# Optimization experiments

Hardware: AMD Instinct MI355X
Metric: run time of the kernel (lower is better)

Reference implementation:

```python
import math
import jax, jax.numpy as jnp
import numpy as np

# ---------- static Cl(3,0,0) algebra tables ----------
_BLADES = [(), (1,), (2,), (3,), (1, 2), (1, 3), (2, 3), (1, 2, 3)]
N_BLADES = 8
SUBSPACES = np.array([1, 3, 3, 1])
GRADE = np.array([len(b) for b in _BLADES])  # blade index -> grade

def _blade_mul(a, b):
    idx = list(a) + list(b)
    sign = 1
    changed = True
    while changed:
        changed = False
        for t in range(len(idx) - 1):
            if idx[t] > idx[t + 1]:
                idx[t], idx[t + 1] = idx[t + 1], idx[t]
                sign = -sign
                changed = True
    out = []
    t = 0
    while t < len(idx):
        if t + 1 < len(idx) and idx[t] == idx[t + 1]:
            t += 2  # e_i e_i = +1 (Euclidean metric)
        else:
            out.append(idx[t]); t += 1
    return sign, tuple(out)

# cayley[i, j, k]: e_i * e_k contributes sign to blade j (matches einsum 'bni,nijk,bnk->bnj')
CAYLEY = np.zeros((N_BLADES, N_BLADES, N_BLADES), dtype=np.float32)
for i, ba in enumerate(_BLADES):
    for k, bb in enumerate(_BLADES):
        s, res = _blade_mul(ba, bb)
        CAYLEY[i, _BLADES.index(res), k] = s

_starts = np.concatenate([[0], np.cumsum(SUBSPACES)[:-1]])
_paths = np.zeros((4, 4, 4), dtype=bool)
for gi in range(4):
    for gj in range(4):
        for gk in range(4):
            si, sj, sk = _starts[gi], _starts[gj], _starts[gk]
            blk = CAYLEY[si:si + SUBSPACES[gi], sj:sj + SUBSPACES[gj], sk:sk + SUBSPACES[gk]]
            _paths[gi, gj, gk] = np.any(blk != 0)
_grade_idx = np.argwhere(_paths)  # row-major order, matches torch.nonzero
N_PATHS = len(_grade_idx)  # 20 for Cl(3,0)

_bi, _bj, _bk, _pidx, _cv = [], [], [], [], []
for p, (gi, gj, gk) in enumerate(_grade_idx):
    for bi in range(_starts[gi], _starts[gi] + SUBSPACES[gi]):
        for bj in range(_starts[gj], _starts[gj] + SUBSPACES[gj]):
            for bk in range(_starts[gk], _starts[gk] + SUBSPACES[gk]):
                c = CAYLEY[bi, bj, bk]
                if c != 0:
                    _bi.append(bi); _bj.append(bj); _bk.append(bk)
                    _pidx.append(p); _cv.append(c)
BI = np.array(_bi); BJ = np.array(_bj); BK = np.array(_bk)
PIDX = np.array(_pidx); CV = np.array(_cv, dtype=np.float32)  # E = 64 nonzero entries

G_ONEHOT = (GRADE[:, None] == np.arange(4)[None, :]).astype(np.float32)  # (8, 4)

B, N_IN, N_OUT = 2048, 512, 512
EPS = 1e-6

def setup_inputs() -> dict:
    key = jax.random.key(0)
    k = jax.random.split(key, 6)
    x = jax.random.normal(k[0], (B, N_IN, N_BLADES), jnp.float32)
    weight = jax.random.normal(k[1], (N_OUT, N_IN, N_PATHS), jnp.float32) / math.sqrt(N_IN * 4)
    w_right = jax.random.normal(k[2], (N_IN, N_IN, 4), jnp.float32) / math.sqrt(N_IN)
    w_left = jax.random.normal(k[3], (N_OUT, N_IN, 4), jnp.float32) / math.sqrt(N_IN)
    b_left = jax.random.normal(k[4], (N_OUT,), jnp.float32) * 0.01
    norm_a = jnp.zeros((1, N_IN, 4), jnp.float32)  # normalization_init = 0
    return dict(x=x, weight=weight, w_right=w_right, w_left=w_left, b_left=b_left, norm_a=norm_a)

def _mvlinear(x, w):
    # w: (out, in, n_grades) -> per-blade weight via grade lookup (repeat_interleave)
    return jnp.einsum('bni,mni->bmi', x, w[:, :, GRADE])

def reference(x, weight, w_right, w_left, b_left, norm_a):
    # linear_right (no bias)
    xr = _mvlinear(x, w_right)
    # NormalizationLayer: per-grade norm, sigmoid-gated rescale toward 1
    norms = jnp.sqrt(jnp.einsum('bni,ig->bng', xr * xr, G_ONEHOT))  # (B, n, 4)
    factor = jax.nn.sigmoid(norm_a) * (norms - 1.0) + 1.0
    xr = xr / (factor[:, :, GRADE] + EPS)
    # sparse bilinear geometric product: only the 64 nonzero cayley entries
    pair = x[:, :, BI] * xr[:, :, BK]            # (B, n, E)
    wsel = weight[:, :, PIDX] * CV               # (m, n, E)
    tmp = jnp.einsum('bne,mne->bme', pair, wsel)  # (B, m, E)
    bilinear = jnp.zeros((x.shape[0], weight.shape[0], N_BLADES), x.dtype).at[:, :, BJ].add(tmp)
    # linear_left with bias embedded on the scalar blade (index 0)
    left = _mvlinear(x, w_left).at[:, :, 0].add(b_left)
    return (left + bilinear) / math.sqrt(2.0)
```

## Files before the change

kernel.cpp:

```cpp
#include <hip/hip_runtime.h>
#include <stdint.h>


#define B_DIM 2048
#define N_DIM 512
#define PLANE (B_DIM * N_DIM)
#define WPLANE (N_DIM * N_DIM)
#define KTOT (9 * N_DIM)
#define LDSP 40

using frag8 = __attribute__((ext_vector_type(8))) short;
using f32x4 = __attribute__((ext_vector_type(4))) float;

__device__ __forceinline__ float bf2f(unsigned short u) {
  union { unsigned int i; float f; } v;
  v.i = ((unsigned int)u) << 16;
  return v.f;
}
__device__ __forceinline__ unsigned short f2bf(float f) {
  unsigned int u = __float_as_uint(f);
  return (unsigned short)((u + 0x7FFFu + ((u >> 16) & 1u)) >> 16);
}
__device__ __forceinline__ unsigned int pairpack(unsigned int a, unsigned int r) {
  const float pe = __uint_as_float(a << 16) * __uint_as_float(r << 16);
  const float po = __uint_as_float(a & 0xFFFF0000u) * __uint_as_float(r & 0xFFFF0000u);
  return __builtin_amdgcn_perm(__float_as_uint(po) + 0x8000u,
                               __float_as_uint(pe) + 0x8000u, 0x07060302u);
}

#define SGN_INIT {                                                     \
  {0,0,0,0,0x8000,0x8000,0x8000,0x8000},                               \
  {0,0,0,0,0x8000,0x8000,0x8000,0x8000},                               \
  {0,0x8000,0,0,0,0,0x8000,0},                                         \
  {0,0x8000,0x8000,0,0x8000,0,0,0x8000},                               \
  {0,0x8000,0,0,0,0,0x8000,0},                                         \
  {0,0x8000,0x8000,0,0x8000,0,0,0x8000},                               \
  {0,0,0x8000,0,0,0x8000,0,0},                                         \
  {0,0,0x8000,0,0,0x8000,0,0} }
#define PJK_INIT {                                                     \
  {0,4,4,4,10,10,10,16},  {5,1,11,11,6,6,17,12},                       \
  {5,11,1,11,6,17,6,12},  {5,11,11,1,17,6,6,12},                       \
  {13,7,7,18,2,14,14,8},  {13,7,18,7,14,2,14,8},                       \
  {13,18,7,7,14,14,2,8},  {19,15,15,15,9,9,9,3} }
#define GR_INIT {0,1,1,1,2,2,2,3}


__global__ __launch_bounds__(256) void repack_x(const float* __restrict__ x,
                                                unsigned short* __restrict__ xt) {
  const int t = blockIdx.x * 256 + threadIdx.x;
  const float4 v0 = *(const float4*)(x + (size_t)t * 8);
  const float4 v1 = *(const float4*)(x + (size_t)t * 8 + 4);
  const float v[8] = {v0.x, v0.y, v0.z, v0.w, v1.x, v1.y, v1.z, v1.w};
#pragma unroll
  for (int i = 0; i < 8; ++i) xt[(size_t)i * PLANE + t] = f2bf(v[i]);
}

__global__ __launch_bounds__(256) void repack_wr(const float* __restrict__ wr,
                                                 unsigned short* __restrict__ wrt) {
  const int t = blockIdx.x * 256 + threadIdx.x;
  const float4 v = *(const float4*)(wr + (size_t)t * 4);
  const float p[4] = {v.x, v.y, v.z, v.w};
#pragma unroll
  for (int g = 0; g < 4; ++g) wrt[(size_t)g * WPLANE + t] = f2bf(p[g]);
}

__global__ __launch_bounds__(256) void build_W(const float* __restrict__ w,
                                               const float* __restrict__ wl,
                                               unsigned short* __restrict__ Wall) {
  constexpr int PJK[8][8] = PJK_INIT;
  constexpr unsigned short SGN[8][8] = SGN_INIT;
  constexpr int GR[8] = GR_INIT;
  const int t = blockIdx.x * 256 + threadIdx.x;
  const int m = t >> 9, n = t & 511;
  const float* wrow = w + (size_t)t * 20;
  const float* wlrow = wl + (size_t)t * 4;
  unsigned short w20[20];
#pragma unroll
  for (int p = 0; p < 20; ++p) w20[p] = f2bf(wrow[p]);
  unsigned short wl4[4];
#pragma unroll
  for (int g = 0; g < 4; ++g) wl4[g] = f2bf(wlrow[g]);
#pragma unroll
  for (int j = 0; j < 8; ++j) {
    const size_t base = ((size_t)j * N_DIM + m) * KTOT + n;
#pragma unroll
    for (int k = 0; k < 8; ++k)
      Wall[base + (size_t)k * N_DIM] = (unsigned short)(w20[PJK[j][k]] ^ SGN[j][k]);
    Wall[base + (size_t)8 * N_DIM] = wl4[GR[j]];
  }
}

__global__ __launch_bounds__(256) void normk(unsigned short* __restrict__ xre,
                                             const float* __restrict__ na) {
  const int t = blockIdx.x * 256 + threadIdx.x;
  const int n = t & 511;
  float v[8];
#pragma unroll
  for (int p = 0; p < 8; ++p) v[p] = bf2f(xre[(size_t)p * PLANE + t]);
  const float n0 = fabsf(v[0]);
  const float n1 = sqrtf(v[1] * v[1] + v[2] * v[2] + v[3] * v[3]);
  const float n2 = sqrtf(v[4] * v[4] + v[5] * v[5] + v[6] * v[6]);
  const float n3 = fabsf(v[7]);
  float f[4];
  const float nm[4] = {n0, n1, n2, n3};
#pragma unroll
  for (int g = 0; g < 4; ++g) {
    const float a = na[n * 4 + g];
    const float sig = 1.0f / (1.0f + __expf(-a));
    f[g] = sig * (nm[g] - 1.0f) + 1.0f + 1e-6f;
  }
  v[0] /= f[0];
  v[1] /= f[1]; v[2] /= f[1]; v[3] /= f[1];
  v[4] /= f[2]; v[5] /= f[2]; v[6] /= f[2];
  v[7] /= f[3];
#pragma unroll
  for (int p = 0; p < 8; ++p) xre[(size_t)p * PLANE + t] = f2bf(v[p]);
  xre[(size_t)8 * PLANE + t] = 0x3F80;
}


__global__ __launch_bounds__(512, 4) void gemm1(const unsigned short* __restrict__ xt,
                                                const unsigned short* __restrict__ wrt,
                                                unsigned short* __restrict__ xre) {
  constexpr int GR[8] = GR_INIT;
  __shared__ unsigned short sA[2][128 * LDSP];
  __shared__ unsigned short sB[2][128 * LDSP];
  const int bm0 = blockIdx.x * 128, bn0 = blockIdx.y * 128, z = blockIdx.z;
  const unsigned short* A = xt + (size_t)z * PLANE;
  const unsigned short* Bm = wrt + (size_t)GR[z] * WPLANE;
  unsigned short* C = xre + (size_t)z * PLANE;

  const int tid = (int)threadIdx.x;
  const int lane = tid & 63, wave = tid >> 6;
  const int wm = (wave >> 2) * 64, wn = (wave & 3) * 32;
  const int fr = lane & 15, quad = lane >> 4;
  const int row = tid >> 2, k8 = (tid & 3) * 8;

  f32x4 acc[4][2];
#pragma unroll
  for (int mt = 0; mt < 4; ++mt)
#pragma unroll
    for (int nt = 0; nt < 2; ++nt) acc[mt][nt] = (f32x4){0.f, 0.f, 0.f, 0.f};

  const unsigned short* pa = A + (size_t)(bm0 + row) * N_DIM + k8;
  const unsigned short* pb = Bm + (size_t)(bn0 + row) * N_DIM + k8;
  uint4 va = *(const uint4*)pa;
  uint4 vb = *(const uint4*)pb;

  for (int it = 0; it < 16; ++it) {
    const int cur = it & 1;
    *(uint4*)&sA[cur][row * LDSP + k8] = va;
    *(uint4*)&sB[cur][row * LDSP + k8] = vb;
    if (it + 1 < 16) {
      va = *(const uint4*)(pa + (it + 1) * 32);
      vb = *(const uint4*)(pb + (it + 1) * 32);
    }
    __syncthreads();
    frag8 af[4], bf2r[2];
#pragma unroll
    for (int t = 0; t < 4; ++t)
      af[t] = *(const frag8*)&sA[cur][(wm + t * 16 + fr) * LDSP + quad * 8];
#pragma unroll
    for (int t = 0; t < 2; ++t)
      bf2r[t] = *(const frag8*)&sB[cur][(wn + t * 16 + fr) * LDSP + quad * 8];
#pragma unroll
    for (int mt = 0; mt < 4; ++mt)
#pragma unroll
      for (int nt = 0; nt < 2; ++nt)
        acc[mt][nt] = __builtin_amdgcn_mfma_f32_16x16x32_bf16(af[mt], bf2r[nt], acc[mt][nt], 0, 0, 0);
  }
#pragma unroll
  for (int mt = 0; mt < 4; ++mt) {
    const int row0 = bm0 + wm + mt * 16 + quad * 4;
#pragma unroll
    for (int nt = 0; nt < 2; ++nt) {
      const int col = bn0 + wn + nt * 16 + fr;
#pragma unroll
      for (int r = 0; r < 4; ++r)
        C[(size_t)(row0 + r) * N_DIM + col] = f2bf(acc[mt][nt][r]);
    }
  }
}


__global__ __launch_bounds__(512, 4) void gemm2(const unsigned short* __restrict__ xt,
                                                const unsigned short* __restrict__ xre,
                                                const unsigned short* __restrict__ Wall,
                                                const float* __restrict__ bl,
                                                float* __restrict__ out) {
  __shared__ unsigned short sA[2][128 * LDSP];
  __shared__ unsigned short sB[2][128 * LDSP];
  const int bm0 = blockIdx.x * 128, bn0 = blockIdx.y * 128, j = blockIdx.z;

  const int tid = (int)threadIdx.x;
  const int lane = tid & 63, wave = tid >> 6;
  const int wm = (wave >> 2) * 64, wn = (wave & 3) * 32;
  const int fr = lane & 15, quad = lane >> 4;
  const int row = tid >> 2, k8 = (tid & 3) * 8;
  const int pj = (j == 3 || j == 4) ? (j ^ 7) : j;

  f32x4 acc[4][2];
#pragma unroll
  for (int mt = 0; mt < 4; ++mt)
#pragma unroll
    for (int nt = 0; nt < 2; ++nt) acc[mt][nt] = (f32x4){0.f, 0.f, 0.f, 0.f};

  const size_t arow = (size_t)(bm0 + row) * N_DIM + k8;
  const size_t wrowo = ((size_t)j * N_DIM + bn0 + row) * KTOT + k8;

  auto ieof = [&](int sl) -> int {
    int ps = (sl == 3 || sl == 4) ? (sl ^ 7) : sl;
    int ix = pj ^ ps;
    ix = (ix == 3 || ix == 4) ? (ix ^ 7) : ix;
    return (sl == 8) ? j : ix;
  };

  uint4 rx = *(const uint4*)(xt + (size_t)ieof(0) * PLANE + arow);
  uint4 rr = *(const uint4*)(xre + arow);
  uint4 rw = *(const uint4*)(Wall + wrowo);

  for (int it = 0; it < 144; ++it) {
    const int cur = it & 1;
    uint4 o;
    o.x = pairpack(rx.x, rr.x);
    o.y = pairpack(rx.y, rr.y);
    o.z = pairpack(rx.z, rr.z);
    o.w = pairpack(rx.w, rr.w);
    *(uint4*)&sA[cur][row * LDSP + k8] = o;
    *(uint4*)&sB[cur][row * LDSP + k8] = rw;
    if (it + 1 < 144) {
      const int itn = it + 1;
      const int sl = itn >> 4, n0 = (itn & 15) * 32;
      const int ie = ieof(sl);
      rx = *(const uint4*)(xt + (size_t)ie * PLANE + arow + n0);
      rr = *(const uint4*)(xre + (size_t)sl * PLANE + arow + n0);
      rw = *(const uint4*)(Wall + wrowo + (size_t)sl * N_DIM + n0);
    }
    __syncthreads();
    frag8 af[4], bf2r[2];
#pragma unroll
    for (int t = 0; t < 4; ++t)
      af[t] = *(const frag8*)&sA[cur][(wm + t * 16 + fr) * LDSP + quad * 8];
#pragma unroll
    for (int t = 0; t < 2; ++t)
      bf2r[t] = *(const frag8*)&sB[cur][(wn + t * 16 + fr) * LDSP + quad * 8];
#pragma unroll
    for (int mt = 0; mt < 4; ++mt)
#pragma unroll
      for (int nt = 0; nt < 2; ++nt)
        acc[mt][nt] = __builtin_amdgcn_mfma_f32_16x16x32_bf16(af[mt], bf2r[nt], acc[mt][nt], 0, 0, 0);
  }

  const float inv = 0.70710678118654752f;
#pragma unroll
  for (int nt = 0; nt < 2; ++nt) {
    const int col = bn0 + wn + nt * 16 + fr;
    const float bias = (j == 0) ? bl[col] : 0.0f;
#pragma unroll
    for (int mt = 0; mt < 4; ++mt) {
      const int row0 = bm0 + wm + mt * 16 + quad * 4;
#pragma unroll
      for (int r = 0; r < 4; ++r)
        out[((size_t)(row0 + r) * N_DIM + col) * 8 + j] =
            (acc[mt][nt][r] + bias) * inv;
    }
  }
}


extern "C" void kernel_launch(void* const* d_in, const int* in_sizes, int n_in,
                              void* d_out, int out_size, void* d_ws, size_t ws_size,
                              hipStream_t stream) {
  const float* x = (const float*)d_in[0];
  const float* w = (const float*)d_in[1];
  const float* wr = (const float*)d_in[2];
  const float* wl = (const float*)d_in[3];
  const float* bl = (const float*)d_in[4];
  const float* na = (const float*)d_in[5];
  float* out = (float*)d_out;

  char* ws = (char*)d_ws;
  unsigned short* xt = (unsigned short*)(ws);
  unsigned short* xre = (unsigned short*)(ws + 16777216);
  unsigned short* wrt = (unsigned short*)(ws + 35651584);
  unsigned short* Wall = (unsigned short*)(ws + 37748736);

  repack_x<<<4096, 256, 0, stream>>>(x, xt);
  repack_wr<<<1024, 256, 0, stream>>>(wr, wrt);
  build_W<<<1024, 256, 0, stream>>>(w, wl, Wall);
  gemm1<<<dim3(16, 4, 8), 512, 0, stream>>>(xt, wrt, xre);
  normk<<<4096, 256, 0, stream>>>(xre, na);
  gemm2<<<dim3(16, 4, 8), 512, 0, stream>>>(xt, xre, Wall, bl, out);
}
```

Measured before the change: 289.2 us.

## Use direct global-to-LDS loads with XOR-swizzled tiles and triple-buffered weights

Both GEMM kernels now stage operand tiles with global_load_lds, writing straight into LDS and skipping the register round trip. Padded LDS rows are replaced by a dense 32-wide layout with an XOR swizzle to avoid bank conflicts. gemm2 triple-buffers the weight tile and moves the pair-product packing after the MFMAs so loads overlap compute, using custom waitcnt/barrier fences. The risks are in the swizzle/fence correctness and the fact that the LDS-load lane-to-address mapping has to match the swizzled layout.

Measured after the change: 309.7 us. 1.07x slower.

```diff
diff --git a/kernel.cpp b/kernel.cpp
--- a/kernel.cpp
+++ b/kernel.cpp
@@ -7,7 +7,7 @@
 #define PLANE (B_DIM * N_DIM)
 #define WPLANE (N_DIM * N_DIM)
 #define KTOT (9 * N_DIM)
-#define LDSP 40
+#define TILE_US (128 * 32)
 
 using frag8 = __attribute__((ext_vector_type(8))) short;
 using f32x4 = __attribute__((ext_vector_type(4))) float;
@@ -27,6 +27,19 @@
   return __builtin_amdgcn_perm(__float_as_uint(po) + 0x8000u,
                                __float_as_uint(pe) + 0x8000u, 0x07060302u);
 }
+
+typedef const unsigned int __attribute__((address_space(1)))* gas_t;
+typedef unsigned int __attribute__((address_space(3)))* las_t;
+__device__ __forceinline__ void gload16(const void* g, void* l) {
+  __builtin_amdgcn_global_load_lds((gas_t)g, (las_t)l, 16, 0, 0);
+}
+
+#define PIPE_FENCE(N)                                                  \
+  do {                                                                 \
+    asm volatile("s_waitcnt vmcnt(" #N ") lgkmcnt(0)" ::: "memory");   \
+    __builtin_amdgcn_s_barrier();                                      \
+    __builtin_amdgcn_sched_barrier(0);                                 \
+  } while (0)
 
 #define SGN_INIT {                                                     \
   {0,0,0,0,0x8000,0x8000,0x8000,0x8000},                               \
@@ -123,18 +136,87 @@
                                                 const unsigned short* __restrict__ wrt,
                                                 unsigned short* __restrict__ xre) {
   constexpr int GR[8] = GR_INIT;
-  __shared__ unsigned short sA[2][128 * LDSP];
-  __shared__ unsigned short sB[2][128 * LDSP];
+  __shared__ unsigned short sA[2][TILE_US];
+  __shared__ unsigned short sB[2][TILE_US];
   const int bm0 = blockIdx.x * 128, bn0 = blockIdx.y * 128, z = blockIdx.z;
   const unsigned short* A = xt + (size_t)z * PLANE;
   const unsigned short* Bm = wrt + (size_t)GR[z] * WPLANE;
   unsigned short* C = xre + (size_t)z * PLANE;
+
+  const int tid = (int)threadIdx.x;
+  const int lane = tid & 63, wave = tid >> 6;
+  const int wm = (wave >> 2) * 64, wn = (wave & 3) * 32;
+  const int fr = lane & 15, quad = lane >> 4;
+  const int row = tid >> 2;
+  const int ks = (((tid & 3) ^ ((tid >> 3) & 3))) * 8;
+  const int wbase = wave * 512;
+
+  const unsigned short* pa = A + (size_t)(bm0 + row) * N_DIM + ks;
+  const unsigned short* pb = Bm + (size_t)(bn0 + row) * N_DIM + ks;
+
+  const int msw = (fr >> 1) & 3;
+  const int rdA = (wm + fr) * 32 + (quad ^ msw) * 8;
+  const int rdB = (wn + fr) * 32 + (quad ^ msw) * 8;
+
+  f32x4 acc[4][2];
+#pragma unroll
+  for (int mt = 0; mt < 4; ++mt)
+#pragma unroll
+    for (int nt = 0; nt < 2; ++nt) acc[mt][nt] = (f32x4){0.f, 0.f, 0.f, 0.f};
+
+  gload16(pa, &sA[0][wbase]);
+  gload16(pb, &sB[0][wbase]);
+  PIPE_FENCE(0);
+
+  for (int it = 0; it < 16; ++it) {
+    const int c = it & 1;
+    if (it < 15) {
+      gload16(pa + ((it + 1) << 5), &sA[c ^ 1][wbase]);
+      gload16(pb + ((it + 1) << 5), &sB[c ^ 1][wbase]);
+    }
+    frag8 af[4], bfr[2];
+#pragma unroll
+    for (int t = 0; t < 4; ++t) af[t] = *(const frag8*)&sA[c][rdA + t * 512];
+#pragma unroll
+    for (int t = 0; t < 2; ++t) bfr[t] = *(const frag8*)&sB[c][rdB + t * 512];
+#pragma unroll
+    for (int mt = 0; mt < 4; ++mt)
+#pragma unroll
+      for (int nt = 0; nt < 2; ++nt)
+        acc[mt][nt] = __builtin_amdgcn_mfma_f32_16x16x32_bf16(af[mt], bfr[nt], acc[mt][nt], 0, 0, 0);
+    if (it < 15) PIPE_FENCE(0);
+  }
+#pragma unroll
+  for (int mt = 0; mt < 4; ++mt) {
+    const int row0 = bm0 + wm + mt * 16 + quad * 4;
+#pragma unroll
+    for (int nt = 0; nt < 2; ++nt) {
+      const int col = bn0 + wn + nt * 16 + fr;
+#pragma unroll
+      for (int r = 0; r < 4; ++r)
+        C[(size_t)(row0 + r) * N_DIM + col] = f2bf(acc[mt][nt][r]);
+    }
+  }
+}
+
+
+__global__ __launch_bounds__(512, 4) void gemm2(const unsigned short* __restrict__ xt,
+                                                const unsigned short* __restrict__ xre,
+                                                const unsigned short* __restrict__ Wall,
+                                                const float* __restrict__ bl,
+                                                float* __restrict__ out) {
+  __shared__ unsigned short sA[2][TILE_US];
+  __shared__ unsigned short sB3[3][TILE_US];
+  const int bm0 = blockIdx.x * 128, bn0 = blockIdx.y * 128, j = blockIdx.z;
 
   const int tid = (int)threadIdx.x;
   const int lane = tid & 63, wave = tid >> 6;
   const int wm = (wave >> 2) * 64, wn = (wave & 3) * 32;
   const int fr = lane & 15, quad = lane >> 4;
   const int row = tid >> 2, k8 = (tid & 3) * 8;
+  const int ks = (((tid & 3) ^ ((tid >> 3) & 3))) * 8;
+  const int wbase = wave * 512;
+  const int pj = (j == 3 || j == 4) ? (j ^ 7) : j;
 
   f32x4 acc[4][2];
 #pragma unroll
@@ -142,71 +224,8 @@
 #pragma unroll
     for (int nt = 0; nt < 2; ++nt) acc[mt][nt] = (f32x4){0.f, 0.f, 0.f, 0.f};
 
-  const unsigned short* pa = A + (size_t)(bm0 + row) * N_DIM + k8;
-  const unsigned short* pb = Bm + (size_t)(bn0 + row) * N_DIM + k8;
-  uint4 va = *(const uint4*)pa;
-  uint4 vb = *(const uint4*)pb;
-
-  for (int it = 0; it < 16; ++it) {
-    const int cur = it & 1;
-    *(uint4*)&sA[cur][row * LDSP + k8] = va;
-    *(uint4*)&sB[cur][row * LDSP + k8] = vb;
-    if (it + 1 < 16) {
-      va = *(const uint4*)(pa + (it + 1) * 32);
-      vb = *(const uint4*)(pb + (it + 1) * 32);
-    }
-    __syncthreads();
-    frag8 af[4], bf2r[2];
-#pragma unroll
-    for (int t = 0; t < 4; ++t)
-      af[t] = *(const frag8*)&sA[cur][(wm + t * 16 + fr) * LDSP + quad * 8];
-#pragma unroll
-    for (int t = 0; t < 2; ++t)
-      bf2r[t] = *(const frag8*)&sB[cur][(wn + t * 16 + fr) * LDSP + quad * 8];
-#pragma unroll
-    for (int mt = 0; mt < 4; ++mt)
-#pragma unroll
-      for (int nt = 0; nt < 2; ++nt)
-        acc[mt][nt] = __builtin_amdgcn_mfma_f32_16x16x32_bf16(af[mt], bf2r[nt], acc[mt][nt], 0, 0, 0);
-  }
-#pragma unroll
-  for (int mt = 0; mt < 4; ++mt) {
-    const int row0 = bm0 + wm + mt * 16 + quad * 4;
-#pragma unroll
-    for (int nt = 0; nt < 2; ++nt) {
-      const int col = bn0 + wn + nt * 16 + fr;
-#pragma unroll
-      for (int r = 0; r < 4; ++r)
-        C[(size_t)(row0 + r) * N_DIM + col] = f2bf(acc[mt][nt][r]);
-    }
-  }
-}
-
-
-__global__ __launch_bounds__(512, 4) void gemm2(const unsigned short* __restrict__ xt,
-                                                const unsigned short* __restrict__ xre,
-                                                const unsigned short* __restrict__ Wall,
-                                                const float* __restrict__ bl,
-                                                float* __restrict__ out) {
-  __shared__ unsigned short sA[2][128 * LDSP];
-  __shared__ unsigned short sB[2][128 * LDSP];
-  const int bm0 = blockIdx.x * 128, bn0 = blockIdx.y * 128, j = blockIdx.z;
-
-  const int tid = (int)threadIdx.x;
-  const int lane = tid & 63, wave = tid >> 6;
-  const int wm = (wave >> 2) * 64, wn = (wave & 3) * 32;
-  const int fr = lane & 15, quad = lane >> 4;
-  const int row = tid >> 2, k8 = (tid & 3) * 8;
-  const int pj = (j == 3 || j == 4) ? (j ^ 7) : j;
-
-  f32x4 acc[4][2];
-#pragma unroll
-  for (int mt = 0; mt < 4; ++mt)
-#pragma unroll
-    for (int nt = 0; nt < 2; ++nt) acc[mt][nt] = (f32x4){0.f, 0.f, 0.f, 0.f};
-
   const size_t arow = (size_t)(bm0 + row) * N_DIM + k8;
-  const size_t wrowo = ((size_t)j * N_DIM + bn0 + row) * KTOT + k8;
+  const unsigned short* pwb = Wall + ((size_t)j * N_DIM + bn0 + row) * KTOT + ks;
 
   auto ieof = [&](int sl) -> int {
     int ps = (sl == 3 || sl == 4) ? (sl ^ 7) : sl;
@@ -215,40 +234,61 @@
     return (sl == 8) ? j : ix;
   };
 
-  uint4 rx = *(const uint4*)(xt + (size_t)ieof(0) * PLANE + arow);
-  uint4 rr = *(const uint4*)(xre + arow);
-  uint4 rw = *(const uint4*)(Wall + wrowo);
-
-  for (int it = 0; it < 144; ++it) {
-    const int cur = it & 1;
+  const int msw = (fr >> 1) & 3;
+  const int rdA = (wm + fr) * 32 + (quad ^ msw) * 8;
+  const int rdB = (wn + fr) * 32 + (quad ^ msw) * 8;
+  const int wrA = row * 32 + ks;
+
+  {
+    uint4 rx = *(const uint4*)(xt + ((size_t)ieof(0) << 20) + arow);
+    uint4 rr = *(const uint4*)(xre + arow);
+    gload16(pwb, &sB3[0][wbase]);
+    gload16(pwb + 32, &sB3[1][wbase]);
     uint4 o;
     o.x = pairpack(rx.x, rr.x);
     o.y = pairpack(rx.y, rr.y);
     o.z = pairpack(rx.z, rr.z);
     o.w = pairpack(rx.w, rr.w);
-    *(uint4*)&sA[cur][row * LDSP + k8] = o;
-    *(uint4*)&sB[cur][row * LDSP + k8] = rw;
-    if (it + 1 < 144) {
-      const int itn = it + 1;
-      const int sl = itn >> 4, n0 = (itn & 15) * 32;
-      const int ie = ieof(sl);
-      rx = *(const uint4*)(xt + (size_t)ie * PLANE + arow + n0);
-      rr = *(const uint4*)(xre + (size_t)sl * PLANE + arow + n0);
-      rw = *(const uint4*)(Wall + wrowo + (size_t)sl * N_DIM + n0);
-    }
-    __syncthreads();
-    frag8 af[4], bf2r[2];
-#pragma unroll
-    for (int t = 0; t < 4; ++t)
-      af[t] = *(const frag8*)&sA[cur][(wm + t * 16 + fr) * LDSP + quad * 8];
-#pragma unroll
-    for (int t = 0; t < 2; ++t)
-      bf2r[t] = *(const frag8*)&sB[cur][(wn + t * 16 + fr) * LDSP + quad * 8];
+    *(uint4*)&sA[0][wrA] = o;
+  }
+  PIPE_FENCE(1);
+
+  uint4 rx, rr;
+  int cb = 0, wb = 2;
+  for (int it = 0; it < 144; ++it) {
+    const int c2 = it & 1;
+    if (it < 143) {
+      const int kn = it + 1;
+      const int slk = kn >> 4, n0k = (kn & 15) << 5;
+      int ps = (slk == 3 || slk == 4) ? (slk ^ 7) : slk;
+      int ix = pj ^ ps;
+      ix = (ix == 3 || ix == 4) ? (ix ^ 7) : ix;
+      const int ie = (slk == 8) ? j : ix;
+      rx = *(const uint4*)(xt + ((size_t)ie << 20) + arow + n0k);
+      rr = *(const uint4*)(xre + ((size_t)slk << 20) + arow + n0k);
+      if (it < 142) gload16(pwb + (size_t)(it + 2) * 32, &sB3[wb][wbase]);
+    }
+    frag8 af[4], bfr[2];
+#pragma unroll
+    for (int t = 0; t < 4; ++t) af[t] = *(const frag8*)&sA[c2][rdA + t * 512];
+#pragma unroll
+    for (int t = 0; t < 2; ++t) bfr[t] = *(const frag8*)&sB3[cb][rdB + t * 512];
 #pragma unroll
     for (int mt = 0; mt < 4; ++mt)
 #pragma unroll
       for (int nt = 0; nt < 2; ++nt)
-        acc[mt][nt] = __builtin_amdgcn_mfma_f32_16x16x32_bf16(af[mt], bf2r[nt], acc[mt][nt], 0, 0, 0);
+        acc[mt][nt] = __builtin_amdgcn_mfma_f32_16x16x32_bf16(af[mt], bfr[nt], acc[mt][nt], 0, 0, 0);
+    if (it < 143) {
+      uint4 o;
+      o.x = pairpack(rx.x, rr.x);
+      o.y = pairpack(rx.y, rr.y);
+      o.z = pairpack(rx.z, rr.z);
+      o.w = pairpack(rx.w, rr.w);
+      *(uint4*)&sA[c2 ^ 1][wrA] = o;
+      PIPE_FENCE(1);
+    }
+    cb = (cb + 1 == 3) ? 0 : cb + 1;
+    wb = (wb + 1 == 3) ? 0 : wb + 1;
   }
 
   const float inv = 0.70710678118654752f;
```

## Use direct global-to-LDS loads with swizzled layout and 4-wave 64x64 warp tiles

Applied to the files above, without the earlier changes.

Both GEMM kernels switch from register-staged global loads plus padded LDS to global_load_lds direct transfers into an XOR-swizzled, unpadded LDS layout. Blocks go from 8 to 4 waves, each computing a 64x64 tile (16 MFMAs per k-step instead of 8), which raises MFMA work per LDS fragment read. In gemm2 the weight tile streams directly into LDS, while the pair-product A tile is loaded early and packed after the MFMAs, so prefetch overlaps compute with one barrier per step. The cost is higher register pressure from 64 accumulator floats per lane, fewer waves per block, and reliance on the swizzle matching how global_load_lds places each lane's data.

After: 307.8 us. 1.06x slower.

```diff
diff --git a/kernel.cpp b/kernel.cpp
--- a/kernel.cpp
+++ b/kernel.cpp
@@ -7,7 +7,6 @@
 #define PLANE (B_DIM * N_DIM)
 #define WPLANE (N_DIM * N_DIM)
 #define KTOT (9 * N_DIM)
-#define LDSP 40
 
 using frag8 = __attribute__((ext_vector_type(8))) short;
 using f32x4 = __attribute__((ext_vector_type(4))) float;
@@ -26,6 +25,12 @@
   const float po = __uint_as_float(a & 0xFFFF0000u) * __uint_as_float(r & 0xFFFF0000u);
   return __builtin_amdgcn_perm(__float_as_uint(po) + 0x8000u,
                                __float_as_uint(pe) + 0x8000u, 0x07060302u);
+}
+
+typedef const unsigned int __attribute__((address_space(1)))* gas_t;
+typedef unsigned int __attribute__((address_space(3)))* las_t;
+__device__ __forceinline__ void gload16(const void* g, void* l) {
+  __builtin_amdgcn_global_load_lds((gas_t)g, (las_t)l, 16, 0, 0);
 }
 
 #define SGN_INIT {                                                     \
@@ -119,61 +124,70 @@
 }
 
 
-__global__ __launch_bounds__(512, 4) void gemm1(const unsigned short* __restrict__ xt,
+__global__ __launch_bounds__(256, 3) void gemm1(const unsigned short* __restrict__ xt,
                                                 const unsigned short* __restrict__ wrt,
                                                 unsigned short* __restrict__ xre) {
   constexpr int GR[8] = GR_INIT;
-  __shared__ unsigned short sA[2][128 * LDSP];
-  __shared__ unsigned short sB[2][128 * LDSP];
+  __shared__ __attribute__((aligned(16))) unsigned short sA[2][4096];
+  __shared__ __attribute__((aligned(16))) unsigned short sB[2][4096];
   const int bm0 = blockIdx.x * 128, bn0 = blockIdx.y * 128, z = blockIdx.z;
   const unsigned short* A = xt + (size_t)z * PLANE;
   const unsigned short* Bm = wrt + (size_t)GR[z] * WPLANE;
   unsigned short* C = xre + (size_t)z * PLANE;
 
   const int tid = (int)threadIdx.x;
-  const int lane = tid & 63, wave = tid >> 6;
-  const int wm = (wave >> 2) * 64, wn = (wave & 3) * 32;
-  const int fr = lane & 15, quad = lane >> 4;
-  const int row = tid >> 2, k8 = (tid & 3) * 8;
-
-  f32x4 acc[4][2];
+  const int l = tid & 63, w = tid >> 6;
+  const int wm = (w >> 1) * 64, wn = (w & 1) * 64;
+  const int fr = l & 15, quad = l >> 4, msw = (fr >> 1) & 3;
+  const int rdA = (wm + fr) * 32 + (quad ^ msw) * 8;
+  const int rdB = (wn + fr) * 32 + (quad ^ msw) * 8;
+  const int ks = (((l & 3) ^ ((l >> 3) & 3))) * 8;
+  const int r0 = w * 32 + (l >> 2);
+  const unsigned short* pa0 = A + (size_t)(bm0 + r0) * N_DIM + ks;
+  const unsigned short* pa1 = pa0 + (size_t)16 * N_DIM;
+  const unsigned short* pb0 = Bm + (size_t)(bn0 + r0) * N_DIM + ks;
+  const unsigned short* pb1 = pb0 + (size_t)16 * N_DIM;
+  const int db = w * 1024;
+
+  f32x4 acc[4][4];
 #pragma unroll
   for (int mt = 0; mt < 4; ++mt)
 #pragma unroll
-    for (int nt = 0; nt < 2; ++nt) acc[mt][nt] = (f32x4){0.f, 0.f, 0.f, 0.f};
-
-  const unsigned short* pa = A + (size_t)(bm0 + row) * N_DIM + k8;
-  const unsigned short* pb = Bm + (size_t)(bn0 + row) * N_DIM + k8;
-  uint4 va = *(const uint4*)pa;
-  uint4 vb = *(const uint4*)pb;
-
+    for (int nt = 0; nt < 4; ++nt) acc[mt][nt] = (f32x4){0.f, 0.f, 0.f, 0.f};
+
+  gload16(pa0, &sA[0][db]);
+  gload16(pa1, &sA[0][db + 512]);
+  gload16(pb0, &sB[0][db]);
+  gload16(pb1, &sB[0][db + 512]);
+  __syncthreads();
+
+#pragma unroll 2
   for (int it = 0; it < 16; ++it) {
     const int cur = it & 1;
-    *(uint4*)&sA[cur][row * LDSP + k8] = va;
-    *(uint4*)&sB[cur][row * LDSP + k8] = vb;
-    if (it + 1 < 16) {
-      va = *(const uint4*)(pa + (it + 1) * 32);
-      vb = *(const uint4*)(pb + (it + 1) * 32);
-    }
+    if (it < 15) {
+      const int off = (it + 1) * 32;
+      gload16(pa0 + off, &sA[cur ^ 1][db]);
+      gload16(pa1 + off, &sA[cur ^ 1][db + 512]);
+      gload16(pb0 + off, &sB[cur ^ 1][db]);
+      gload16(pb1 + off, &sB[cur ^ 1][db + 512]);
+    }
+    frag8 af[4], bf[4];
+#pragma unroll
+    for (int t = 0; t < 4; ++t) af[t] = *(const frag8*)&sA[cur][rdA + t * 512];
+#pragma unroll
+    for (int t = 0; t < 4; ++t) bf[t] = *(const frag8*)&sB[cur][rdB + t * 512];
+#pragma unroll
+    for (int mt = 0; mt < 4; ++mt)
+#pragma unroll
+      for (int nt = 0; nt < 4; ++nt)
+        acc[mt][nt] = __builtin_amdgcn_mfma_f32_16x16x32_bf16(af[mt], bf[nt], acc[mt][nt], 0, 0, 0);
     __syncthreads();
-    frag8 af[4], bf2r[2];
-#pragma unroll
-    for (int t = 0; t < 4; ++t)
-      af[t] = *(const frag8*)&sA[cur][(wm + t * 16 + fr) * LDSP + quad * 8];
-#pragma unroll
-    for (int t = 0; t < 2; ++t)
-      bf2r[t] = *(const frag8*)&sB[cur][(wn + t * 16 + fr) * LDSP + quad * 8];
-#pragma unroll
-    for (int mt = 0; mt < 4; ++mt)
-#pragma unroll
-      for (int nt = 0; nt < 2; ++nt)
-        acc[mt][nt] = __builtin_amdgcn_mfma_f32_16x16x32_bf16(af[mt], bf2r[nt], acc[mt][nt], 0, 0, 0);
   }
 #pragma unroll
   for (int mt = 0; mt < 4; ++mt) {
     const int row0 = bm0 + wm + mt * 16 + quad * 4;
 #pragma unroll
-    for (int nt = 0; nt < 2; ++nt) {
+    for (int nt = 0; nt < 4; ++nt) {
       const int col = bn0 + wn + nt * 16 + fr;
 #pragma unroll
       for (int r = 0; r < 4; ++r)
@@ -183,30 +197,31 @@
 }
 
 
-__global__ __launch_bounds__(512, 4) void gemm2(const unsigned short* __restrict__ xt,
+__global__ __launch_bounds__(256, 3) void gemm2(const unsigned short* __restrict__ xt,
                                                 const unsigned short* __restrict__ xre,
                                                 const unsigned short* __restrict__ Wall,
                                                 const float* __restrict__ bl,
                                                 float* __restrict__ out) {
-  __shared__ unsigned short sA[2][128 * LDSP];
-  __shared__ unsigned short sB[2][128 * LDSP];
+  __shared__ __attribute__((aligned(16))) unsigned short sA[2][4096];
+  __shared__ __attribute__((aligned(16))) unsigned short sB[2][4096];
   const int bm0 = blockIdx.x * 128, bn0 = blockIdx.y * 128, j = blockIdx.z;
 
   const int tid = (int)threadIdx.x;
-  const int lane = tid & 63, wave = tid >> 6;
-  const int wm = (wave >> 2) * 64, wn = (wave & 3) * 32;
-  const int fr = lane & 15, quad = lane >> 4;
-  const int row = tid >> 2, k8 = (tid & 3) * 8;
+  const int l = tid & 63, w = tid >> 6;
+  const int wm = (w >> 1) * 64, wn = (w & 1) * 64;
+  const int fr = l & 15, quad = l >> 4, msw = (fr >> 1) & 3;
+  const int rdA = (wm + fr) * 32 + (quad ^ msw) * 8;
+  const int rdB = (wn + fr) * 32 + (quad ^ msw) * 8;
+  const int ks = (((l & 3) ^ ((l >> 3) & 3))) * 8;
+  const int r0 = w * 32 + (l >> 2);
+  const int db = w * 1024;
   const int pj = (j == 3 || j == 4) ? (j ^ 7) : j;
 
-  f32x4 acc[4][2];
-#pragma unroll
-  for (int mt = 0; mt < 4; ++mt)
-#pragma unroll
-    for (int nt = 0; nt < 2; ++nt) acc[mt][nt] = (f32x4){0.f, 0.f, 0.f, 0.f};
-
-  const size_t arow = (size_t)(bm0 + row) * N_DIM + k8;
-  const size_t wrowo = ((size_t)j * N_DIM + bn0 + row) * KTOT + k8;
+  const size_t ar0 = (size_t)(bm0 + r0) * N_DIM + (l & 3) * 8;
+  const size_t ar1 = ar0 + (size_t)16 * N_DIM;
+  const int wr0 = r0 * 32 + ks, wr1 = wr0 + 512;
+  const unsigned short* pw0 = Wall + ((size_t)j * N_DIM + bn0 + r0) * KTOT + ks;
+  const unsigned short* pw1 = pw0 + (size_t)16 * KTOT;
 
   auto ieof = [&](int sl) -> int {
     int ps = (sl == 3 || sl == 4) ? (sl ^ 7) : sl;
@@ -215,45 +230,75 @@
     return (sl == 8) ? j : ix;
   };
 
-  uint4 rx = *(const uint4*)(xt + (size_t)ieof(0) * PLANE + arow);
-  uint4 rr = *(const uint4*)(xre + arow);
-  uint4 rw = *(const uint4*)(Wall + wrowo);
-
+  f32x4 acc[4][4];
+#pragma unroll
+  for (int mt = 0; mt < 4; ++mt)
+#pragma unroll
+    for (int nt = 0; nt < 4; ++nt) acc[mt][nt] = (f32x4){0.f, 0.f, 0.f, 0.f};
+
+  {
+    const unsigned short* bx = xt + ((size_t)ieof(0)) * PLANE;
+    const uint4 x0 = *(const uint4*)(bx + ar0);
+    const uint4 e0 = *(const uint4*)(xre + ar0);
+    const uint4 x1 = *(const uint4*)(bx + ar1);
+    const uint4 e1 = *(const uint4*)(xre + ar1);
+    gload16(pw0, &sB[0][db]);
+    gload16(pw1, &sB[0][db + 512]);
+    uint4 o0, o1;
+    o0.x = pairpack(x0.x, e0.x); o0.y = pairpack(x0.y, e0.y);
+    o0.z = pairpack(x0.z, e0.z); o0.w = pairpack(x0.w, e0.w);
+    o1.x = pairpack(x1.x, e1.x); o1.y = pairpack(x1.y, e1.y);
+    o1.z = pairpack(x1.z, e1.z); o1.w = pairpack(x1.w, e1.w);
+    *(uint4*)&sA[0][wr0] = o0;
+    *(uint4*)&sA[0][wr1] = o1;
+  }
+  __syncthreads();
+
+#pragma unroll 2
   for (int it = 0; it < 144; ++it) {
     const int cur = it & 1;
-    uint4 o;
-    o.x = pairpack(rx.x, rr.x);
-    o.y = pairpack(rx.y, rr.y);
-    o.z = pairpack(rx.z, rr.z);
-    o.w = pairpack(rx.w, rr.w);
-    *(uint4*)&sA[cur][row * LDSP + k8] = o;
-    *(uint4*)&sB[cur][row * LDSP + k8] = rw;
-    if (it + 1 < 144) {
-      const int itn = it + 1;
-      const int sl = itn >> 4, n0 = (itn & 15) * 32;
-      const int ie = ieof(sl);
-      rx = *(const uint4*)(xt + (size_t)ie * PLANE + arow + n0);
-      rr = *(const uint4*)(xre + (size_t)sl * PLANE + arow + n0);
-      rw = *(const uint4*)(Wall + wrowo + (size_t)sl * N_DIM + n0);
+    uint4 x0, e0, x1, e1;
+    if (it < 143) {
+      const int kn = it + 1;
+      const int sl = kn >> 4, n0 = (kn & 15) << 5;
+      int ps = (sl == 3 || sl == 4) ? (sl ^ 7) : sl;
+      int ix = pj ^ ps;
+      ix = (ix == 3 || ix == 4) ? (ix ^ 7) : ix;
+      const int ie = (sl == 8) ? j : ix;
+      const unsigned short* bx = xt + (size_t)ie * PLANE;
+      const unsigned short* be = xre + (size_t)sl * PLANE;
+      x0 = *(const uint4*)(bx + ar0 + n0);
+      e0 = *(const uint4*)(be + ar0 + n0);
+      x1 = *(const uint4*)(bx + ar1 + n0);
+      e1 = *(const uint4*)(be + ar1 + n0);
+      gload16(pw0 + (size_t)kn * 32, &sB[cur ^ 1][db]);
+      gload16(pw1 + (size_t)kn * 32, &sB[cur ^ 1][db + 512]);
+    }
+    frag8 af[4], bf[4];
+#pragma unroll
+    for (int t = 0; t < 4; ++t) af[t] = *(const frag8*)&sA[cur][rdA + t * 512];
+#pragma unroll
+    for (int t = 0; t < 4; ++t) bf[t] = *(const frag8*)&sB[cur][rdB + t * 512];
+#pragma unroll
+    for (int mt = 0; mt < 4; ++mt)
+#pragma unroll
+      for (int nt = 0; nt < 4; ++nt)
+        acc[mt][nt] = __builtin_amdgcn_mfma_f32_16x16x32_bf16(af[mt], bf[nt], acc[mt][nt], 0, 0, 0);
+    if (it < 143) {
+      uint4 o0, o1;
+      o0.x = pairpack(x0.x, e0.x); o0.y = pairpack(x0.y, e0.y);
+      o0.z = pairpack(x0.z, e0.z); o0.w = pairpack(x0.w, e0.w);
+      o1.x = pairpack(x1.x, e1.x); o1.y = pairpack(x1.y, e1.y);
+      o1.z = pairpack(x1.z, e1.z); o1.w = pairpack(x1.w, e1.w);
+      *(uint4*)&sA[cur ^ 1][wr0] = o0;
+      *(uint4*)&sA[cur ^ 1][wr1] = o1;
     }
     __syncthreads();
-    frag8 af[4], bf2r[2];
-#pragma unroll
-    for (int t = 0; t < 4; ++t)
-      af[t] = *(const frag8*)&sA[cur][(wm + t * 16 + fr) * LDSP + quad * 8];
-#pragma unroll
-    for (int t = 0; t < 2; ++t)
-      bf2r[t] = *(const frag8*)&sB[cur][(wn + t * 16 + fr) * LDSP + quad * 8];
-#pragma unroll
-    for (int mt = 0; mt < 4; ++mt)
-#pragma unroll
-      for (int nt = 0; nt < 2; ++nt)
-        acc[mt][nt] = __builtin_amdgcn_mfma_f32_16x16x32_bf16(af[mt], bf2r[nt], acc[mt][nt], 0, 0, 0);
   }
 
   const float inv = 0.70710678118654752f;
 #pragma unroll
-  for (int nt = 0; nt < 2; ++nt) {
+  for (int nt = 0; nt < 4; ++nt) {
     const int col = bn0 + wn + nt * 16 + fr;
     const float bias = (j == 0) ? bl[col] : 0.0f;
 #pragma unroll
@@ -288,7 +333,7 @@
   repack_x<<<4096, 256, 0, stream>>>(x, xt);
   repack_wr<<<1024, 256, 0, stream>>>(wr, wrt);
   build_W<<<1024, 256, 0, stream>>>(w, wl, Wall);
-  gemm1<<<dim3(16, 4, 8), 512, 0, stream>>>(xt, wrt, xre);
+  gemm1<<<dim3(16, 4, 8), 256, 0, stream>>>(xt, wrt, xre);
   normk<<<4096, 256, 0, stream>>>(xre, na);
-  gemm2<<<dim3(16, 4, 8), 512, 0, stream>>>(xt, xre, Wall, bl, out);
-}
+  gemm2<<<dim3(16, 4, 8), 256, 0, stream>>>(xt, xre, Wall, bl, out);
+}
```
